# Kernel optimization log

Hardware: AMD Instinct MI355X
Metric: run time of the kernel (lower is better)

## Reference

```python
import jax, jax.numpy as jnp
import numpy as np

EPS = 1e-5

def _bn_relu(x, gamma, beta):
    # BatchNorm2d in training mode: biased batch stats over (B, H, W)
    mu = jnp.mean(x, axis=(0, 2, 3), keepdims=True)
    var = jnp.mean((x - mu) ** 2, axis=(0, 2, 3), keepdims=True)
    xh = (x - mu) * jax.lax.rsqrt(var + EPS)
    return jax.nn.relu(xh * gamma[None, :, None, None] + beta[None, :, None, None])

def setup_inputs() -> dict:
    key = jax.random.key(0)
    ks = jax.random.split(key, 16)
    B, N, D = 4, 256, 256            # in_channels = 2*D = 512
    feats = jax.random.normal(ks[0], (B, 1 + 2 * N, D), dtype=jnp.float32)
    def lin(k, o, c):
        return jax.random.normal(k, (o, c), dtype=jnp.float32) * (1.0 / np.sqrt(c))
    return {
        "feats": feats,
        "W1": lin(ks[1], 256, 512), "b1": jnp.zeros((256,), jnp.float32),
        "g1": jnp.ones((256,), jnp.float32), "be1": jnp.zeros((256,), jnp.float32),
        "W2": lin(ks[2], 128, 256), "b2": jnp.zeros((128,), jnp.float32),
        "g2": jnp.ones((128,), jnp.float32), "be2": jnp.zeros((128,), jnp.float32),
        "W3": lin(ks[3], 64, 128), "b3": jnp.zeros((64,), jnp.float32),
        "g3": jnp.ones((64,), jnp.float32), "be3": jnp.zeros((64,), jnp.float32),
        "W4": lin(ks[4], 1, 64), "b4": jnp.zeros((1,), jnp.float32),
    }

def reference(feats, W1, b1, g1, be1, W2, b2, g2, be2, W3, b3, g3, be3, W4, b4):
    B, T, Dfull = feats.shape
    f = feats[:, 1:]                                  # [B, 2N, D]
    N = f.shape[1] // 2
    D = f.shape[2]
    f = f.reshape(B, N, 2, D).mean(axis=2)            # [B, N, D]
    fc = jnp.transpose(f, (0, 2, 1))                  # [B, D, N]
    # conv1(cat(x, t)) fused: first D input channels see f_i, last D see f_j
    a = jnp.einsum('oc,bcn->bon', W1[:, :D], fc)      # [B, 256, N]
    bpart = jnp.einsum('oc,bcn->bon', W1[:, D:], fc)  # [B, 256, N]
    h = a[:, :, :, None] + bpart[:, :, None, :] + b1[None, :, None, None]  # [B,256,N,N]
    h = _bn_relu(h, g1, be1)
    h = jnp.einsum('oc,bcij->boij', W2, h) + b2[None, :, None, None]
    h = _bn_relu(h, g2, be2)
    h = jnp.einsum('oc,bcij->boij', W3, h) + b3[None, :, None, None]
    h = _bn_relu(h, g3, be3)
    h = jnp.einsum('oc,bcij->boij', W4, h) + b4[None, :, None, None]
    return h[:, 0]                                    # [B, N, N]
```

## Files before the change

### kernel.cpp

```cpp
#include <hip/hip_runtime.h>
#include <hip/hip_bf16.h>

#define EPS 1e-5f

typedef __attribute__((ext_vector_type(8))) short bf16x8;
typedef __attribute__((ext_vector_type(4))) float f32x4;

static constexpr size_t OFF_FT    = 0;
static constexpr size_t OFF_W1T   = 1048576;
static constexpr size_t OFF_W2B   = 1572864;
static constexpr size_t OFF_W3B   = 1638400;
static constexpr size_t OFF_S1    = 1654784;
static constexpr size_t OFF_T1    = 1655808;
static constexpr size_t OFF_S2    = 1658368;
static constexpr size_t OFF_T2    = 1658880;
static constexpr size_t OFF_S3    = 1659392;
static constexpr size_t OFF_T3    = 1659648;
static constexpr size_t OFF_ST2   = 1660928;
static constexpr size_t OFF_ST3   = 1669120;
static constexpr size_t OFF_ABT   = 1703936;
static constexpr size_t OFF_H2T   = 4194304;
static constexpr size_t OFF_P1    = OFF_H2T;
static constexpr size_t OFF_H3T   = 71303168;

static __device__ inline float bfu2f(unsigned int u16) {
    return __uint_as_float(u16 << 16);
}
static __device__ inline unsigned short f2bfu(float f) {
    unsigned int u = __float_as_uint(f);
    unsigned int r = u + 0x7fffu + ((u >> 16) & 1u);
    return (unsigned short)(r >> 16);
}
static __device__ inline unsigned int pkbf(float lo, float hi) {
    __hip_bfloat162 p = __float22bfloat162_rn(make_float2(lo, hi));
    return *reinterpret_cast<unsigned int*>(&p);
}

__global__ void k0_pairmean_T(const float* __restrict__ feats, float* __restrict__ fT) {
    __shared__ float s[64][65];
    int b = blockIdx.x >> 2;
    int n0 = (blockIdx.x & 3) * 64;
    int tid = threadIdx.x;
    const float* fb = feats + (size_t)b * 513 * 256;
    for (int c0 = 0; c0 < 256; c0 += 64) {
        for (int idx = tid; idx < 64 * 64; idx += 256) {
            int n = idx >> 6, c = idx & 63;
            const float* r = fb + (size_t)(1 + 2 * (n0 + n)) * 256 + c0 + c;
            s[n][c] = 0.5f * (r[0] + r[256]);
        }
        __syncthreads();
        for (int idx = tid; idx < 64 * 64; idx += 256) {
            int c = idx >> 6, n = idx & 63;
            fT[((size_t)b * 256 + c0 + c) * 256 + n0 + n] = s[n][c];
        }
        __syncthreads();
    }
}

__global__ void kt_prep(const float* __restrict__ W1, const float* __restrict__ W2,
                        const float* __restrict__ W3, float* __restrict__ W1T,
                        unsigned short* __restrict__ W2b, unsigned short* __restrict__ W3b) {
    int idx = blockIdx.x * 256 + threadIdx.x;
    if (idx < 131072) {
        int c = idx >> 9, o = idx & 511;
        W1T[idx] = (o < 256) ? W1[(size_t)o * 512 + c] : W1[(size_t)(o - 256) * 512 + 256 + c];
    } else if (idx < 163840) {
        int j = idx - 131072;
        W2b[j] = f2bfu(W2[j]);
    } else if (idx < 172032) {
        int j = idx - 163840;
        W3b[j] = f2bfu(W3[j]);
    }
}

__global__ __launch_bounds__(256) void k1_gemm(const float* __restrict__ W1T,
                                               const float* __restrict__ fT,
                                               float* __restrict__ abT,
                                               float2* __restrict__ part) {
    __shared__ float sW[64][68];
    __shared__ float sF[64][68];
    int tid = threadIdx.x;
    int b = blockIdx.x >> 2, n0 = (blockIdx.x & 3) * 64;
    int o0 = blockIdx.y * 64;
    int jq = tid & 15, og = tid >> 4;
    float acc[4][4] = {};
    for (int c0 = 0; c0 < 256; c0 += 64) {
        for (int idx = tid; idx < 64 * 64; idx += 256) {
            int c = idx >> 6, o = idx & 63;
            sW[c][o] = W1T[(size_t)(c0 + c) * 512 + o0 + o];
        }
        for (int idx = tid; idx < 64 * 64; idx += 256) {
            int c = idx >> 6, n = idx & 63;
            sF[c][n] = fT[((size_t)b * 256 + c0 + c) * 256 + n0 + n];
        }
        __syncthreads();
        #pragma unroll 8
        for (int c = 0; c < 64; ++c) {
            float4 rv = *(const float4*)&sF[c][jq * 4];
            float4 wv = *(const float4*)&sW[c][og * 4];
            float rr[4] = {rv.x, rv.y, rv.z, rv.w};
            float ww[4] = {wv.x, wv.y, wv.z, wv.w};
            #pragma unroll
            for (int m = 0; m < 4; ++m)
                #pragma unroll
                for (int w = 0; w < 4; ++w) acc[m][w] += ww[m] * rr[w];
        }
        __syncthreads();
    }
    for (int w = 0; w < 4; ++w) {
        int n = n0 + jq * 4 + w;
        float4 v = {acc[0][w], acc[1][w], acc[2][w], acc[3][w]};
        *(float4*)&abT[((size_t)(b * 256) + n) * 512 + o0 + og * 4] = v;
    }
    #pragma unroll
    for (int m = 0; m < 4; ++m) {
        float s = 0.f, q = 0.f;
        #pragma unroll
        for (int w = 0; w < 4; ++w) { float v = acc[m][w]; s += v; q += v * v; }
        #pragma unroll
        for (int off = 8; off; off >>= 1) { s += __shfl_down(s, off); q += __shfl_down(q, off); }
        if (jq == 0) part[(size_t)blockIdx.x * 512 + o0 + og * 4 + m] = make_float2(s, q);
    }
}

__global__ void k1b_stats(const float2* __restrict__ part, const float* __restrict__ g1,
                          const float* __restrict__ be1, float* __restrict__ s1,
                          float* __restrict__ t1) {
    __shared__ float Sl[4][512], Ql[4][512];
    int o = threadIdx.x;
    for (int b = 0; b < 4; ++b) {
        float s = 0.f, q = 0.f;
        #pragma unroll
        for (int nt = 0; nt < 4; ++nt) {
            float2 p = part[(size_t)(b * 4 + nt) * 512 + o];
            s += p.x; q += p.y;
        }
        Sl[b][o] = s; Ql[b][o] = q;
    }
    __syncthreads();
    if (o < 256) {
        float msum = 0.f, e2sum = 0.f;
        #pragma unroll
        for (int b = 0; b < 4; ++b) {
            float ma = Sl[b][o] * (1.f / 256.f), mb = Sl[b][o + 256] * (1.f / 256.f);
            msum += ma + mb;
            e2sum += Ql[b][o] * (1.f / 256.f) + Ql[b][o + 256] * (1.f / 256.f) + 2.f * ma * mb;
        }
        float m = msum * 0.25f, e2 = e2sum * 0.25f;
        float var = e2 - m * m;
        float s = g1[o] * rsqrtf(var + EPS);
        s1[o] = s;
        t1[o] = be1[o] - m * s;
    }
}

__global__ __launch_bounds__(256) void k2_mfma(const float* __restrict__ abT,
                                               const unsigned short* __restrict__ W2b,
                                               const float* __restrict__ s1,
                                               const float* __restrict__ t1,
                                               unsigned short* __restrict__ h2T,
                                               float* __restrict__ gS2,
                                               float* __restrict__ gQ2) {
    __shared__ __align__(16) char smem[39936];
    float* aaS = (float*)smem;
    float* ssS = (float*)(smem + 1024);
    unsigned short* sW = (unsigned short*)(smem + 2048);
    unsigned short* sB = (unsigned short*)(smem + 20480);
    float* sS = (float*)(smem + 38912);
    float* sQ = (float*)(smem + 39424);
    unsigned short* sT = (unsigned short*)smem;

    int tid = threadIdx.x;
    int j0 = blockIdx.x * 128, i = blockIdx.y, b = blockIdx.z;

    {
        float av = abT[((size_t)(b * 256 + i)) * 512 + tid];
        float s = s1[tid];
        aaS[tid] = fmaf(av, s, t1[tid]);
        ssS[tid] = s;
    }
    if (tid < 128) { sS[tid] = 0.f; sQ[tid] = 0.f; }
    __syncthreads();

    int lane = tid & 63, wv = tid >> 6;
    int wr = wv >> 1, wc = wv & 1;
    int lo = lane & 15, khi = lane >> 4;

    f32x4 acc[4][4] = {};
    const float* bpB = abT + ((size_t)(b * 256 + j0)) * 512 + 256;

    for (int c0 = 0; c0 < 256; c0 += 64) {
        #pragma unroll
        for (int k = 0; k < 4; ++k) {
            int f = tid + k * 256; int o = f >> 3, cs = f & 7;
            uint4 v = *(const uint4*)(W2b + o * 256 + c0 + cs * 8);
            *(uint4*)(sW + o * 72 + cs * 8) = v;
        }
        #pragma unroll
        for (int k = 0; k < 8; ++k) {
            int f = tid + k * 256; int j = f >> 4, cs = f & 15;
            float4 bp = *(const float4*)(bpB + (size_t)j * 512 + c0 + cs * 4);
            float4 a4 = *(const float4*)&aaS[c0 + cs * 4];
            float4 s4 = *(const float4*)&ssS[c0 + cs * 4];
            float r0 = fmaxf(fmaf(bp.x, s4.x, a4.x), 0.f);
            float r1 = fmaxf(fmaf(bp.y, s4.y, a4.y), 0.f);
            float r2 = fmaxf(fmaf(bp.z, s4.z, a4.z), 0.f);
            float r3 = fmaxf(fmaf(bp.w, s4.w, a4.w), 0.f);
            *(uint2*)(sB + j * 72 + cs * 4) = make_uint2(pkbf(r0, r1), pkbf(r2, r3));
        }
        __syncthreads();
        const unsigned short* aB = sW + (wr * 64 + lo) * 72 + khi * 8;
        const unsigned short* bB = sB + (wc * 64 + lo) * 72 + khi * 8;
        #pragma unroll
        for (int ks = 0; ks < 2; ++ks) {
            bf16x8 af[4], bfr[4];
            #pragma unroll
            for (int fm = 0; fm < 4; ++fm) af[fm] = *(const bf16x8*)(aB + fm * 16 * 72 + ks * 32);
            #pragma unroll
            for (int fn = 0; fn < 4; ++fn) bfr[fn] = *(const bf16x8*)(bB + fn * 16 * 72 + ks * 32);
            #pragma unroll
            for (int fm = 0; fm < 4; ++fm)
                #pragma unroll
                for (int fn = 0; fn < 4; ++fn)
                    acc[fm][fn] = __builtin_amdgcn_mfma_f32_16x16x32_bf16(af[fm], bfr[fn], acc[fm][fn], 0, 0, 0);
        }
        __syncthreads();
    }

    #pragma unroll
    for (int fm = 0; fm < 4; ++fm)
        #pragma unroll
        for (int r = 0; r < 4; ++r) {
            float s = 0.f, q = 0.f;
            #pragma unroll
            for (int fn = 0; fn < 4; ++fn) { float v = acc[fm][fn][r]; s += v; q += v * v; }
            #pragma unroll
            for (int off = 8; off; off >>= 1) { s += __shfl_down(s, off); q += __shfl_down(q, off); }
            if (lo == 0) {
                int o = wr * 64 + fm * 16 + khi * 4 + r;
                atomicAdd(&sS[o], s);
                atomicAdd(&sQ[o], q);
            }
        }
    __syncthreads();

    #pragma unroll
    for (int fm = 0; fm < 4; ++fm)
        #pragma unroll
        for (int fn = 0; fn < 4; ++fn) {
            int oq = wr * 64 + fm * 16 + khi * 4;
            int j  = wc * 64 + fn * 16 + lo;
            unsigned int u0 = pkbf(acc[fm][fn][0], acc[fm][fn][1]);
            unsigned int u1 = pkbf(acc[fm][fn][2], acc[fm][fn][3]);
            *(uint2*)(sT + j * 136 + oq) = make_uint2(u0, u1);
        }
    __syncthreads();
    {
        int jrow = tid >> 1, half = tid & 1;
        size_t gbase = (((size_t)(b * 256 + i)) * 256 + j0 + jrow) * 128 + half * 64;
        #pragma unroll
        for (int e = 0; e < 8; ++e) {
            uint4 v = *(const uint4*)(sT + jrow * 136 + half * 64 + e * 8);
            *(uint4*)(h2T + gbase + e * 8) = v;
        }
    }
    if (tid < 128) {
        int slot = (i & 7) * 128;
        atomicAdd(&gS2[slot + tid], sS[tid]);
        atomicAdd(&gQ2[slot + tid], sQ[tid]);
    }
}

__global__ void kbnparam(const float* __restrict__ gS, const float* __restrict__ gQ,
                         const float* __restrict__ g, const float* __restrict__ be,
                         float* __restrict__ s, float* __restrict__ t, int C, float invc) {
    int o = threadIdx.x;
    if (o < C) {
        float su = 0.f, qu = 0.f;
        #pragma unroll
        for (int k = 0; k < 8; ++k) { su += gS[k * C + o]; qu += gQ[k * C + o]; }
        float mean = su * invc;
        float var = qu * invc - mean * mean;
        float sc = g[o] * rsqrtf(var + EPS);
        s[o] = sc;
        t[o] = be[o] - mean * sc;
    }
}

__global__ __launch_bounds__(256) void k3_mfma(const unsigned short* __restrict__ h2T,
                                               const unsigned short* __restrict__ W3b,
                                               const float* __restrict__ s2,
                                               const float* __restrict__ t2,
                                               unsigned short* __restrict__ h3T,
                                               float* __restrict__ gS3,
                                               float* __restrict__ gQ3) {
    __shared__ __align__(16) char smem[39424];
    float* s2S = (float*)smem;
    float* t2S = (float*)(smem + 512);
    unsigned short* sW3 = (unsigned short*)(smem + 1024);
    unsigned short* sB  = (unsigned short*)(smem + 18432);
    float* sS = (float*)(smem + 38912);
    float* sQ = (float*)(smem + 39168);
    unsigned short* sT  = (unsigned short*)(smem + 1024);

    int tid = threadIdx.x;
    int i = blockIdx.x, b = blockIdx.y;
    if (tid < 128) { s2S[tid] = s2[tid]; t2S[tid] = t2[tid]; }
    if (tid < 64) { sS[tid] = 0.f; sQ[tid] = 0.f; }
    {
        int o = tid >> 2, qd = tid & 3;
        #pragma unroll
        for (int e = 0; e < 4; ++e) {
            uint4 v = *(const uint4*)(W3b + o * 128 + qd * 32 + e * 8);
            *(uint4*)(sW3 + o * 136 + qd * 32 + e * 8) = v;
        }
    }
    __syncthreads();

    int lane = tid & 63, wv = tid >> 6;
    int lo = lane & 15, khi = lane >> 4;

    f32x4 acc[4][4] = {};
    const unsigned short* src = h2T + (((size_t)(b * 256 + i)) * 256 + tid) * 128;

    for (int c0 = 0; c0 < 128; c0 += 32) {
        #pragma unroll
        for (int e = 0; e < 4; ++e) {
            uint4 v = *(const uint4*)(src + c0 + e * 8);
            int c = c0 + e * 8;
            float4 sa = *(const float4*)&s2S[c];
            float4 sb = *(const float4*)&s2S[c + 4];
            float4 ta = *(const float4*)&t2S[c];
            float4 tb = *(const float4*)&t2S[c + 4];
            float r0 = fmaxf(fmaf(bfu2f(v.x & 0xffffu), sa.x, ta.x), 0.f);
            float r1 = fmaxf(fmaf(bfu2f(v.x >> 16),     sa.y, ta.y), 0.f);
            float r2 = fmaxf(fmaf(bfu2f(v.y & 0xffffu), sa.z, ta.z), 0.f);
            float r3 = fmaxf(fmaf(bfu2f(v.y >> 16),     sa.w, ta.w), 0.f);
            float r4 = fmaxf(fmaf(bfu2f(v.z & 0xffffu), sb.x, tb.x), 0.f);
            float r5 = fmaxf(fmaf(bfu2f(v.z >> 16),     sb.y, tb.y), 0.f);
            float r6 = fmaxf(fmaf(bfu2f(v.w & 0xffffu), sb.z, tb.z), 0.f);
            float r7 = fmaxf(fmaf(bfu2f(v.w >> 16),     sb.w, tb.w), 0.f);
            *(uint4*)(sB + tid * 40 + e * 8) =
                make_uint4(pkbf(r0, r1), pkbf(r2, r3), pkbf(r4, r5), pkbf(r6, r7));
        }
        __syncthreads();
        bf16x8 af[4], bfr[4];
        #pragma unroll
        for (int fm = 0; fm < 4; ++fm)
            af[fm] = *(const bf16x8*)(sW3 + (fm * 16 + lo) * 136 + c0 + khi * 8);
        #pragma unroll
        for (int fn = 0; fn < 4; ++fn)
            bfr[fn] = *(const bf16x8*)(sB + (wv * 64 + fn * 16 + lo) * 40 + khi * 8);
        #pragma unroll
        for (int fm = 0; fm < 4; ++fm)
            #pragma unroll
            for (int fn = 0; fn < 4; ++fn)
                acc[fm][fn] = __builtin_amdgcn_mfma_f32_16x16x32_bf16(af[fm], bfr[fn], acc[fm][fn], 0, 0, 0);
        __syncthreads();
    }

    #pragma unroll
    for (int fm = 0; fm < 4; ++fm)
        #pragma unroll
        for (int r = 0; r < 4; ++r) {
            float s = 0.f, q = 0.f;
            #pragma unroll
            for (int fn = 0; fn < 4; ++fn) { float v = acc[fm][fn][r]; s += v; q += v * v; }
            #pragma unroll
            for (int off = 8; off; off >>= 1) { s += __shfl_down(s, off); q += __shfl_down(q, off); }
            if (lo == 0) {
                int o = fm * 16 + khi * 4 + r;
                atomicAdd(&sS[o], s);
                atomicAdd(&sQ[o], q);
            }
        }
    __syncthreads();

    #pragma unroll
    for (int fm = 0; fm < 4; ++fm)
        #pragma unroll
        for (int fn = 0; fn < 4; ++fn) {
            int oq = fm * 16 + khi * 4;
            int j  = wv * 64 + fn * 16 + lo;
            unsigned int u0 = pkbf(acc[fm][fn][0], acc[fm][fn][1]);
            unsigned int u1 = pkbf(acc[fm][fn][2], acc[fm][fn][3]);
            *(uint2*)(sT + j * 72 + oq) = make_uint2(u0, u1);
        }
    __syncthreads();
    {
        size_t gbase = (((size_t)(b * 256 + i)) * 256 + tid) * 64;
        #pragma unroll
        for (int e = 0; e < 8; ++e) {
            uint4 v = *(const uint4*)(sT + tid * 72 + e * 8);
            *(uint4*)(h3T + gbase + e * 8) = v;
        }
    }
    if (tid < 64) {
        int slot = (i & 7) * 64;
        atomicAdd(&gS3[slot + tid], sS[tid]);
        atomicAdd(&gQ3[slot + tid], sQ[tid]);
    }
}

__global__ __launch_bounds__(256) void k4_final(const unsigned short* __restrict__ h3T,
                                                const float* __restrict__ W4,
                                                const float* __restrict__ s3,
                                                const float* __restrict__ t3,
                                                const float* __restrict__ b4,
                                                float* __restrict__ out) {
    __shared__ __align__(16) char smem[37632];
    float* wS = (float*)smem;
    float* sS = (float*)(smem + 256);
    float* tS = (float*)(smem + 512);
    unsigned short* sL = (unsigned short*)(smem + 768);
    int tid = threadIdx.x;
    int i = blockIdx.x, b = blockIdx.y;
    if (tid < 64) { wS[tid] = W4[tid]; sS[tid] = s3[tid]; tS[tid] = t3[tid]; }
    const unsigned short* src = h3T + ((size_t)(b * 256 + i)) * 256 * 64;
    #pragma unroll
    for (int e = 0; e < 8; ++e) {
        int f = tid + 256 * e;
        uint4 v = *(const uint4*)(src + f * 8);
        *(uint4*)(sL + (f >> 3) * 72 + (f & 7) * 8) = v;
    }
    __syncthreads();
    float acc = 0.f;
    #pragma unroll
    for (int e = 0; e < 8; ++e) {
        uint4 v = *(const uint4*)(sL + tid * 72 + e * 8);
        unsigned int w[4] = {v.x, v.y, v.z, v.w};
        #pragma unroll
        for (int k = 0; k < 4; ++k) {
            int c = e * 8 + 2 * k;
            float f0 = bfu2f(w[k] & 0xffffu);
            float f1 = bfu2f(w[k] >> 16);
            acc += wS[c] * fmaxf(fmaf(f0, sS[c], tS[c]), 0.f);
            acc += wS[c + 1] * fmaxf(fmaf(f1, sS[c + 1], tS[c + 1]), 0.f);
        }
    }
    out[((size_t)(b * 256 + i)) * 256 + tid] = acc + b4[0];
}

extern "C" void kernel_launch(void* const* d_in, const int* in_sizes, int n_in,
                              void* d_out, int out_size, void* d_ws, size_t ws_size,
                              hipStream_t stream) {
    const float* feats = (const float*)d_in[0];
    const float* W1  = (const float*)d_in[1];
    const float* g1  = (const float*)d_in[3];
    const float* be1 = (const float*)d_in[4];
    const float* W2  = (const float*)d_in[5];
    const float* g2  = (const float*)d_in[7];
    const float* be2 = (const float*)d_in[8];
    const float* W3  = (const float*)d_in[9];
    const float* g3  = (const float*)d_in[11];
    const float* be3 = (const float*)d_in[12];
    const float* W4  = (const float*)d_in[13];
    const float* b4  = (const float*)d_in[14];

    char* ws = (char*)d_ws;
    float* fT   = (float*)(ws + OFF_FT);
    float* W1T  = (float*)(ws + OFF_W1T);
    unsigned short* W2b = (unsigned short*)(ws + OFF_W2B);
    unsigned short* W3b = (unsigned short*)(ws + OFF_W3B);
    float* abT  = (float*)(ws + OFF_ABT);
    float* s1   = (float*)(ws + OFF_S1);
    float* t1   = (float*)(ws + OFF_T1);
    float* gS2  = (float*)(ws + OFF_ST2);
    float* gQ2  = (float*)(ws + OFF_ST2 + 4096);
    float* gS3  = (float*)(ws + OFF_ST3);
    float* gQ3  = (float*)(ws + OFF_ST3 + 2048);
    float* s2 = (float*)(ws + OFF_S2);
    float* t2 = (float*)(ws + OFF_T2);
    float* s3 = (float*)(ws + OFF_S3);
    float* t3 = (float*)(ws + OFF_T3);
    float2* part = (float2*)(ws + OFF_P1);
    unsigned short* h2T = (unsigned short*)(ws + OFF_H2T);
    unsigned short* h3T = (unsigned short*)(ws + OFF_H3T);
    float* out = (float*)d_out;

    hipMemsetAsync(ws + OFF_ST2, 0, 12288, stream);

    k0_pairmean_T<<<16, 256, 0, stream>>>(feats, fT);
    kt_prep<<<672, 256, 0, stream>>>(W1, W2, W3, W1T, W2b, W3b);
    k1_gemm<<<dim3(16, 8), 256, 0, stream>>>(W1T, fT, abT, part);
    k1b_stats<<<1, 512, 0, stream>>>(part, g1, be1, s1, t1);
    k2_mfma<<<dim3(2, 256, 4), 256, 0, stream>>>(abT, W2b, s1, t1, h2T, gS2, gQ2);
    kbnparam<<<1, 128, 0, stream>>>(gS2, gQ2, g2, be2, s2, t2, 128, 1.f / 262144.f);
    k3_mfma<<<dim3(256, 4), 256, 0, stream>>>(h2T, W3b, s2, t2, h3T, gS3, gQ3);
    kbnparam<<<1, 64, 0, stream>>>(gS3, gQ3, g3, be3, s3, t3, 64, 1.f / 262144.f);
    k4_final<<<dim3(256, 4), 256, 0, stream>>>(h3T, W4, s3, t3, b4, out);
}
```

Before: 241.6 us.

## Double-buffer k2/k3 MFMA loops, load weights from global, split small kernels wider

The k2 and k3 MFMA kernels now double-buffer the BN+ReLU-transformed B tile in LDS. They prefetch the next chunk's activations and weight fragments into registers while the current MFMAs run, and they read weight fragments straight from global memory instead of staging them in shared memory. k3 is split over two j-halves for more blocks, and its LDS footprint shrinks, which should allow higher occupancy. k0 and k1 get more, smaller blocks to fill more CUs. The cost is more global weight traffic, which relies on L2 hits, plus extra register pressure from the prefetched data.

```diff
diff --git a/kernel.cpp b/kernel.cpp
--- a/kernel.cpp
+++ b/kernel.cpp
@@ -36,24 +36,46 @@
     return *reinterpret_cast<unsigned int*>(&p);
 }
 
-__global__ void k0_pairmean_T(const float* __restrict__ feats, float* __restrict__ fT) {
-    __shared__ float s[64][65];
-    int b = blockIdx.x >> 2;
-    int n0 = (blockIdx.x & 3) * 64;
+static __device__ __forceinline__ uint2 bnpk4(float4 fv, const float* aa, const float* ss, int c) {
+    float4 a4 = *(const float4*)(aa + c);
+    float4 s4 = *(const float4*)(ss + c);
+    float r0 = fmaxf(fmaf(fv.x, s4.x, a4.x), 0.f);
+    float r1 = fmaxf(fmaf(fv.y, s4.y, a4.y), 0.f);
+    float r2 = fmaxf(fmaf(fv.z, s4.z, a4.z), 0.f);
+    float r3 = fmaxf(fmaf(fv.w, s4.w, a4.w), 0.f);
+    return make_uint2(pkbf(r0, r1), pkbf(r2, r3));
+}
+static __device__ __forceinline__ uint2 bn2pk4(uint2 v, const float* ss, const float* tt, int c) {
+    float4 s4 = *(const float4*)(ss + c);
+    float4 t4 = *(const float4*)(tt + c);
+    float r0 = fmaxf(fmaf(bfu2f(v.x & 0xffffu), s4.x, t4.x), 0.f);
+    float r1 = fmaxf(fmaf(bfu2f(v.x >> 16),     s4.y, t4.y), 0.f);
+    float r2 = fmaxf(fmaf(bfu2f(v.y & 0xffffu), s4.z, t4.z), 0.f);
+    float r3 = fmaxf(fmaf(bfu2f(v.y >> 16),     s4.w, t4.w), 0.f);
+    return make_uint2(pkbf(r0, r1), pkbf(r2, r3));
+}
+
+__global__ __launch_bounds__(256) void k0_pairmean_T(const float* __restrict__ feats,
+                                                     float* __restrict__ fT) {
+    __shared__ float s[32][65];
+    int bx = blockIdx.x;
+    int b = bx >> 5, nt = (bx >> 2) & 7, ct = bx & 3;
+    int n0 = nt * 32, c0 = ct * 64;
     int tid = threadIdx.x;
     const float* fb = feats + (size_t)b * 513 * 256;
-    for (int c0 = 0; c0 < 256; c0 += 64) {
-        for (int idx = tid; idx < 64 * 64; idx += 256) {
-            int n = idx >> 6, c = idx & 63;
-            const float* r = fb + (size_t)(1 + 2 * (n0 + n)) * 256 + c0 + c;
-            s[n][c] = 0.5f * (r[0] + r[256]);
-        }
-        __syncthreads();
-        for (int idx = tid; idx < 64 * 64; idx += 256) {
-            int c = idx >> 6, n = idx & 63;
-            fT[((size_t)b * 256 + c0 + c) * 256 + n0 + n] = s[n][c];
-        }
-        __syncthreads();
+    #pragma unroll
+    for (int k = 0; k < 8; ++k) {
+        int idx = tid + k * 256;
+        int n = idx >> 6, c = idx & 63;
+        const float* r = fb + (size_t)(1 + 2 * (n0 + n)) * 256 + c0 + c;
+        s[n][c] = 0.5f * (r[0] + r[256]);
+    }
+    __syncthreads();
+    #pragma unroll
+    for (int k = 0; k < 8; ++k) {
+        int idx = tid + k * 256;
+        int c = idx >> 5, n = idx & 31;
+        fT[((size_t)(b * 256) + c0 + c) * 256 + n0 + n] = s[n][c];
     }
 }
 
@@ -77,49 +99,55 @@
                                                const float* __restrict__ fT,
                                                float* __restrict__ abT,
                                                float2* __restrict__ part) {
-    __shared__ float sW[64][68];
+    __shared__ float sW[64][36];
     __shared__ float sF[64][68];
     int tid = threadIdx.x;
-    int b = blockIdx.x >> 2, n0 = (blockIdx.x & 3) * 64;
-    int o0 = blockIdx.y * 64;
-    int jq = tid & 15, og = tid >> 4;
-    float acc[4][4] = {};
+    int bx = blockIdx.x;
+    int b = bx >> 2, n0 = (bx & 3) * 64;
+    int o0 = blockIdx.y * 32;
+    int og = tid >> 4, jq = tid & 15;
+    float acc[2][4] = {};
     for (int c0 = 0; c0 < 256; c0 += 64) {
-        for (int idx = tid; idx < 64 * 64; idx += 256) {
-            int c = idx >> 6, o = idx & 63;
+        #pragma unroll
+        for (int k = 0; k < 8; ++k) {
+            int idx = tid + k * 256;
+            int c = idx >> 5, o = idx & 31;
             sW[c][o] = W1T[(size_t)(c0 + c) * 512 + o0 + o];
         }
-        for (int idx = tid; idx < 64 * 64; idx += 256) {
+        #pragma unroll
+        for (int k = 0; k < 16; ++k) {
+            int idx = tid + k * 256;
             int c = idx >> 6, n = idx & 63;
-            sF[c][n] = fT[((size_t)b * 256 + c0 + c) * 256 + n0 + n];
+            sF[c][n] = fT[((size_t)(b * 256) + c0 + c) * 256 + n0 + n];
         }
         __syncthreads();
         #pragma unroll 8
         for (int c = 0; c < 64; ++c) {
             float4 rv = *(const float4*)&sF[c][jq * 4];
-            float4 wv = *(const float4*)&sW[c][og * 4];
+            float2 wv = *(const float2*)&sW[c][og * 2];
             float rr[4] = {rv.x, rv.y, rv.z, rv.w};
-            float ww[4] = {wv.x, wv.y, wv.z, wv.w};
             #pragma unroll
-            for (int m = 0; m < 4; ++m)
-                #pragma unroll
-                for (int w = 0; w < 4; ++w) acc[m][w] += ww[m] * rr[w];
+            for (int w = 0; w < 4; ++w) {
+                acc[0][w] = fmaf(wv.x, rr[w], acc[0][w]);
+                acc[1][w] = fmaf(wv.y, rr[w], acc[1][w]);
+            }
         }
         __syncthreads();
     }
+    #pragma unroll
     for (int w = 0; w < 4; ++w) {
         int n = n0 + jq * 4 + w;
-        float4 v = {acc[0][w], acc[1][w], acc[2][w], acc[3][w]};
-        *(float4*)&abT[((size_t)(b * 256) + n) * 512 + o0 + og * 4] = v;
-    }
-    #pragma unroll
-    for (int m = 0; m < 4; ++m) {
+        *(float2*)&abT[((size_t)(b * 256) + n) * 512 + o0 + og * 2] =
+            make_float2(acc[0][w], acc[1][w]);
+    }
+    #pragma unroll
+    for (int m = 0; m < 2; ++m) {
         float s = 0.f, q = 0.f;
         #pragma unroll
         for (int w = 0; w < 4; ++w) { float v = acc[m][w]; s += v; q += v * v; }
         #pragma unroll
         for (int off = 8; off; off >>= 1) { s += __shfl_down(s, off); q += __shfl_down(q, off); }
-        if (jq == 0) part[(size_t)blockIdx.x * 512 + o0 + og * 4 + m] = make_float2(s, q);
+        if (jq == 0) part[(size_t)bx * 512 + o0 + og * 2 + m] = make_float2(s, q);
     }
 }
 
@@ -161,14 +189,14 @@
                                                unsigned short* __restrict__ h2T,
                                                float* __restrict__ gS2,
                                                float* __restrict__ gQ2) {
-    __shared__ __align__(16) char smem[39936];
+    __shared__ __align__(16) char smem[23552];
     float* aaS = (float*)smem;
     float* ssS = (float*)(smem + 1024);
-    unsigned short* sW = (unsigned short*)(smem + 2048);
-    unsigned short* sB = (unsigned short*)(smem + 20480);
-    float* sS = (float*)(smem + 38912);
-    float* sQ = (float*)(smem + 39424);
-    unsigned short* sT = (unsigned short*)smem;
+    float* sS  = (float*)(smem + 2048);
+    float* sQ  = (float*)(smem + 2560);
+    unsigned short* sB0 = (unsigned short*)(smem + 3072);
+    unsigned short* sB1 = (unsigned short*)(smem + 13312);
+    unsigned short* sT  = (unsigned short*)(smem + 3072);
 
     int tid = threadIdx.x;
     int j0 = blockIdx.x * 128, i = blockIdx.y, b = blockIdx.z;
@@ -185,46 +213,73 @@
     int lane = tid & 63, wv = tid >> 6;
     int wr = wv >> 1, wc = wv & 1;
     int lo = lane & 15, khi = lane >> 4;
+    int jr = tid >> 1, half = tid & 1;
+
+    const float* bpRow = abT + ((size_t)(b * 256 + j0 + jr)) * 512 + 256 + half * 16;
+    const unsigned short* wBase = W2b + (wr * 64 + lo) * 256 + khi * 8;
 
     f32x4 acc[4][4] = {};
-    const float* bpB = abT + ((size_t)(b * 256 + j0)) * 512 + 256;
-
-    for (int c0 = 0; c0 < 256; c0 += 64) {
-        #pragma unroll
-        for (int k = 0; k < 4; ++k) {
-            int f = tid + k * 256; int o = f >> 3, cs = f & 7;
-            uint4 v = *(const uint4*)(W2b + o * 256 + c0 + cs * 8);
-            *(uint4*)(sW + o * 72 + cs * 8) = v;
-        }
-        #pragma unroll
-        for (int k = 0; k < 8; ++k) {
-            int f = tid + k * 256; int j = f >> 4, cs = f & 15;
-            float4 bp = *(const float4*)(bpB + (size_t)j * 512 + c0 + cs * 4);
-            float4 a4 = *(const float4*)&aaS[c0 + cs * 4];
-            float4 s4 = *(const float4*)&ssS[c0 + cs * 4];
-            float r0 = fmaxf(fmaf(bp.x, s4.x, a4.x), 0.f);
-            float r1 = fmaxf(fmaf(bp.y, s4.y, a4.y), 0.f);
-            float r2 = fmaxf(fmaf(bp.z, s4.z, a4.z), 0.f);
-            float r3 = fmaxf(fmaf(bp.w, s4.w, a4.w), 0.f);
-            *(uint2*)(sB + j * 72 + cs * 4) = make_uint2(pkbf(r0, r1), pkbf(r2, r3));
+    bf16x8 af0, af1, af2, af3;
+
+    {
+        int c = half * 16;
+        float4 f0 = *(const float4*)(bpRow + 0);
+        float4 f1 = *(const float4*)(bpRow + 4);
+        float4 f2 = *(const float4*)(bpRow + 8);
+        float4 f3 = *(const float4*)(bpRow + 12);
+        uint2 p0 = bnpk4(f0, aaS, ssS, c);
+        uint2 p1 = bnpk4(f1, aaS, ssS, c + 4);
+        uint2 p2 = bnpk4(f2, aaS, ssS, c + 8);
+        uint2 p3 = bnpk4(f3, aaS, ssS, c + 12);
+        *(uint4*)(sB0 + jr * 40 + half * 16)     = make_uint4(p0.x, p0.y, p1.x, p1.y);
+        *(uint4*)(sB0 + jr * 40 + half * 16 + 8) = make_uint4(p2.x, p2.y, p3.x, p3.y);
+    }
+    af0 = *(const bf16x8*)(wBase);
+    af1 = *(const bf16x8*)(wBase + 4096);
+    af2 = *(const bf16x8*)(wBase + 8192);
+    af3 = *(const bf16x8*)(wBase + 12288);
+    __syncthreads();
+
+    unsigned short* curB = sB0;
+    unsigned short* nxtB = sB1;
+    #pragma unroll 2
+    for (int k = 0; k < 8; ++k) {
+        int c0 = k * 32;
+        float4 f0, f1, f2, f3;
+        bf16x8 an0, an1, an2, an3;
+        if (k < 7) {
+            f0 = *(const float4*)(bpRow + c0 + 32);
+            f1 = *(const float4*)(bpRow + c0 + 36);
+            f2 = *(const float4*)(bpRow + c0 + 40);
+            f3 = *(const float4*)(bpRow + c0 + 44);
+            an0 = *(const bf16x8*)(wBase + c0 + 32);
+            an1 = *(const bf16x8*)(wBase + 4096 + c0 + 32);
+            an2 = *(const bf16x8*)(wBase + 8192 + c0 + 32);
+            an3 = *(const bf16x8*)(wBase + 12288 + c0 + 32);
+        }
+        bf16x8 bfr[4];
+        #pragma unroll
+        for (int fn = 0; fn < 4; ++fn)
+            bfr[fn] = *(const bf16x8*)(curB + (wc * 64 + fn * 16 + lo) * 40 + khi * 8);
+        #pragma unroll
+        for (int fn = 0; fn < 4; ++fn) {
+            acc[0][fn] = __builtin_amdgcn_mfma_f32_16x16x32_bf16(af0, bfr[fn], acc[0][fn], 0, 0, 0);
+            acc[1][fn] = __builtin_amdgcn_mfma_f32_16x16x32_bf16(af1, bfr[fn], acc[1][fn], 0, 0, 0);
+            acc[2][fn] = __builtin_amdgcn_mfma_f32_16x16x32_bf16(af2, bfr[fn], acc[2][fn], 0, 0, 0);
+            acc[3][fn] = __builtin_amdgcn_mfma_f32_16x16x32_bf16(af3, bfr[fn], acc[3][fn], 0, 0, 0);
+        }
+        if (k < 7) {
+            int cn = c0 + 32 + half * 16;
+            uint2 p0 = bnpk4(f0, aaS, ssS, cn);
+            uint2 p1 = bnpk4(f1, aaS, ssS, cn + 4);
+            uint2 p2 = bnpk4(f2, aaS, ssS, cn + 8);
+            uint2 p3 = bnpk4(f3, aaS, ssS, cn + 12);
+            *(uint4*)(nxtB + jr * 40 + half * 16)     = make_uint4(p0.x, p0.y, p1.x, p1.y);
+            *(uint4*)(nxtB + jr * 40 + half * 16 + 8) = make_uint4(p2.x, p2.y, p3.x, p3.y);
+            af0 = an0; af1 = an1; af2 = an2; af3 = an3;
         }
         __syncthreads();
-        const unsigned short* aB = sW + (wr * 64 + lo) * 72 + khi * 8;
-        const unsigned short* bB = sB + (wc * 64 + lo) * 72 + khi * 8;
-        #pragma unroll
-        for (int ks = 0; ks < 2; ++ks) {
-            bf16x8 af[4], bfr[4];
-            #pragma unroll
-            for (int fm = 0; fm < 4; ++fm) af[fm] = *(const bf16x8*)(aB + fm * 16 * 72 + ks * 32);
-            #pragma unroll
-            for (int fn = 0; fn < 4; ++fn) bfr[fn] = *(const bf16x8*)(bB + fn * 16 * 72 + ks * 32);
-            #pragma unroll
-            for (int fm = 0; fm < 4; ++fm)
-                #pragma unroll
-                for (int fn = 0; fn < 4; ++fn)
-                    acc[fm][fn] = __builtin_amdgcn_mfma_f32_16x16x32_bf16(af[fm], bfr[fn], acc[fm][fn], 0, 0, 0);
-        }
-        __syncthreads();
+        unsigned short* t = curB; curB = nxtB; nxtB = t;
     }
 
     #pragma unroll
@@ -242,26 +297,28 @@
                 atomicAdd(&sQ[o], q);
             }
         }
-    __syncthreads();
-
-    #pragma unroll
-    for (int fm = 0; fm < 4; ++fm)
-        #pragma unroll
-        for (int fn = 0; fn < 4; ++fn) {
-            int oq = wr * 64 + fm * 16 + khi * 4;
-            int j  = wc * 64 + fn * 16 + lo;
-            unsigned int u0 = pkbf(acc[fm][fn][0], acc[fm][fn][1]);
-            unsigned int u1 = pkbf(acc[fm][fn][2], acc[fm][fn][3]);
-            *(uint2*)(sT + j * 136 + oq) = make_uint2(u0, u1);
-        }
-    __syncthreads();
-    {
-        int jrow = tid >> 1, half = tid & 1;
-        size_t gbase = (((size_t)(b * 256 + i)) * 256 + j0 + jrow) * 128 + half * 64;
-        #pragma unroll
-        for (int e = 0; e < 8; ++e) {
-            uint4 v = *(const uint4*)(sT + jrow * 136 + half * 64 + e * 8);
-            *(uint4*)(h2T + gbase + e * 8) = v;
+
+    #pragma unroll
+    for (int rr = 0; rr < 2; ++rr) {
+        __syncthreads();
+        if (wr == rr) {
+            #pragma unroll
+            for (int fm = 0; fm < 4; ++fm)
+                #pragma unroll
+                for (int fn = 0; fn < 4; ++fn) {
+                    int oq = fm * 16 + khi * 4;
+                    int j  = wc * 64 + fn * 16 + lo;
+                    *(uint2*)(sT + j * 72 + oq) =
+                        make_uint2(pkbf(acc[fm][fn][0], acc[fm][fn][1]),
+                                   pkbf(acc[fm][fn][2], acc[fm][fn][3]));
+                }
+        }
+        __syncthreads();
+        size_t g = (((size_t)(b * 256 + i)) * 256 + j0 + jr) * 128 + rr * 64 + half * 32;
+        #pragma unroll
+        for (int e = 0; e < 4; ++e) {
+            uint4 v = *(const uint4*)(sT + jr * 72 + half * 32 + e * 8);
+            *(uint4*)(h2T + g + e * 8) = v;
         }
     }
     if (tid < 128) {
@@ -294,69 +351,86 @@
                                                unsigned short* __restrict__ h3T,
                                                float* __restrict__ gS3,
                                                float* __restrict__ gQ3) {
-    __shared__ __align__(16) char smem[39424];
+    __shared__ __align__(16) char smem[22016];
     float* s2S = (float*)smem;
     float* t2S = (float*)(smem + 512);
-    unsigned short* sW3 = (unsigned short*)(smem + 1024);
-    unsigned short* sB  = (unsigned short*)(smem + 18432);
-    float* sS = (float*)(smem + 38912);
-    float* sQ = (float*)(smem + 39168);
-    unsigned short* sT  = (unsigned short*)(smem + 1024);
+    float* sS  = (float*)(smem + 1024);
+    float* sQ  = (float*)(smem + 1280);
+    unsigned short* sB0 = (unsigned short*)(smem + 1536);
+    unsigned short* sB1 = (unsigned short*)(smem + 11776);
+    unsigned short* sT  = (unsigned short*)(smem + 1536);
 
     int tid = threadIdx.x;
-    int i = blockIdx.x, b = blockIdx.y;
+    int j0 = blockIdx.x * 128, i = blockIdx.y, b = blockIdx.z;
     if (tid < 128) { s2S[tid] = s2[tid]; t2S[tid] = t2[tid]; }
     if (tid < 64) { sS[tid] = 0.f; sQ[tid] = 0.f; }
-    {
-        int o = tid >> 2, qd = tid & 3;
-        #pragma unroll
-        for (int e = 0; e < 4; ++e) {
-            uint4 v = *(const uint4*)(W3b + o * 128 + qd * 32 + e * 8);
-            *(uint4*)(sW3 + o * 136 + qd * 32 + e * 8) = v;
-        }
-    }
     __syncthreads();
 
     int lane = tid & 63, wv = tid >> 6;
     int lo = lane & 15, khi = lane >> 4;
-
-    f32x4 acc[4][4] = {};
-    const unsigned short* src = h2T + (((size_t)(b * 256 + i)) * 256 + tid) * 128;
-
-    for (int c0 = 0; c0 < 128; c0 += 32) {
-        #pragma unroll
-        for (int e = 0; e < 4; ++e) {
-            uint4 v = *(const uint4*)(src + c0 + e * 8);
-            int c = c0 + e * 8;
-            float4 sa = *(const float4*)&s2S[c];
-            float4 sb = *(const float4*)&s2S[c + 4];
-            float4 ta = *(const float4*)&t2S[c];
-            float4 tb = *(const float4*)&t2S[c + 4];
-            float r0 = fmaxf(fmaf(bfu2f(v.x & 0xffffu), sa.x, ta.x), 0.f);
-            float r1 = fmaxf(fmaf(bfu2f(v.x >> 16),     sa.y, ta.y), 0.f);
-            float r2 = fmaxf(fmaf(bfu2f(v.y & 0xffffu), sa.z, ta.z), 0.f);
-            float r3 = fmaxf(fmaf(bfu2f(v.y >> 16),     sa.w, ta.w), 0.f);
-            float r4 = fmaxf(fmaf(bfu2f(v.z & 0xffffu), sb.x, tb.x), 0.f);
-            float r5 = fmaxf(fmaf(bfu2f(v.z >> 16),     sb.y, tb.y), 0.f);
-            float r6 = fmaxf(fmaf(bfu2f(v.w & 0xffffu), sb.z, tb.z), 0.f);
-            float r7 = fmaxf(fmaf(bfu2f(v.w >> 16),     sb.w, tb.w), 0.f);
-            *(uint4*)(sB + tid * 40 + e * 8) =
-                make_uint4(pkbf(r0, r1), pkbf(r2, r3), pkbf(r4, r5), pkbf(r6, r7));
+    int jr = tid >> 1, half = tid & 1;
+
+    const unsigned short* srcRow = h2T + (((size_t)(b * 256 + i)) * 256 + j0 + jr) * 128 + half * 16;
+    const unsigned short* wBase = W3b + lo * 128 + khi * 8;
+
+    f32x4 acc[4][2] = {};
+    bf16x8 af0, af1, af2, af3;
+
+    {
+        int c = half * 16;
+        uint4 v0 = *(const uint4*)(srcRow);
+        uint4 v1 = *(const uint4*)(srcRow + 8);
+        uint2 p0 = bn2pk4(make_uint2(v0.x, v0.y), s2S, t2S, c);
+        uint2 p1 = bn2pk4(make_uint2(v0.z, v0.w), s2S, t2S, c + 4);
+        uint2 p2 = bn2pk4(make_uint2(v1.x, v1.y), s2S, t2S, c + 8);
+        uint2 p3 = bn2pk4(make_uint2(v1.z, v1.w), s2S, t2S, c + 12);
+        *(uint4*)(sB0 + jr * 40 + half * 16)     = make_uint4(p0.x, p0.y, p1.x, p1.y);
+        *(uint4*)(sB0 + jr * 40 + half * 16 + 8) = make_uint4(p2.x, p2.y, p3.x, p3.y);
+    }
+    af0 = *(const bf16x8*)(wBase);
+    af1 = *(const bf16x8*)(wBase + 2048);
+    af2 = *(const bf16x8*)(wBase + 4096);
+    af3 = *(const bf16x8*)(wBase + 6144);
+    __syncthreads();
+
+    unsigned short* curB = sB0;
+    unsigned short* nxtB = sB1;
+    #pragma unroll 2
+    for (int k = 0; k < 4; ++k) {
+        int c0 = k * 32;
+        uint4 v0, v1;
+        bf16x8 an0, an1, an2, an3;
+        if (k < 3) {
+            v0 = *(const uint4*)(srcRow + c0 + 32);
+            v1 = *(const uint4*)(srcRow + c0 + 40);
+            an0 = *(const bf16x8*)(wBase + c0 + 32);
+            an1 = *(const bf16x8*)(wBase + 2048 + c0 + 32);
+            an2 = *(const bf16x8*)(wBase + 4096 + c0 + 32);
+            an3 = *(const bf16x8*)(wBase + 6144 + c0 + 32);
+        }
+        bf16x8 bfr[2];
+        #pragma unroll
+        for (int fn = 0; fn < 2; ++fn)
+            bfr[fn] = *(const bf16x8*)(curB + (wv * 32 + fn * 16 + lo) * 40 + khi * 8);
+        #pragma unroll
+        for (int fn = 0; fn < 2; ++fn) {
+            acc[0][fn] = __builtin_amdgcn_mfma_f32_16x16x32_bf16(af0, bfr[fn], acc[0][fn], 0, 0, 0);
+            acc[1][fn] = __builtin_amdgcn_mfma_f32_16x16x32_bf16(af1, bfr[fn], acc[1][fn], 0, 0, 0);
+            acc[2][fn] = __builtin_amdgcn_mfma_f32_16x16x32_bf16(af2, bfr[fn], acc[2][fn], 0, 0, 0);
+            acc[3][fn] = __builtin_amdgcn_mfma_f32_16x16x32_bf16(af3, bfr[fn], acc[3][fn], 0, 0, 0);
+        }
+        if (k < 3) {
+            int cn = c0 + 32 + half * 16;
+            uint2 p0 = bn2pk4(make_uint2(v0.x, v0.y), s2S, t2S, cn);
+            uint2 p1 = bn2pk4(make_uint2(v0.z, v0.w), s2S, t2S, cn + 4);
+            uint2 p2 = bn2pk4(make_uint2(v1.x, v1.y), s2S, t2S, cn + 8);
+            uint2 p3 = bn2pk4(make_uint2(v1.z, v1.w), s2S, t2S, cn + 12);
+            *(uint4*)(nxtB + jr * 40 + half * 16)     = make_uint4(p0.x, p0.y, p1.x, p1.y);
+            *(uint4*)(nxtB + jr * 40 + half * 16 + 8) = make_uint4(p2.x, p2.y, p3.x, p3.y);
+            af0 = an0; af1 = an1; af2 = an2; af3 = an3;
         }
         __syncthreads();
-        bf16x8 af[4], bfr[4];
-        #pragma unroll
-        for (int fm = 0; fm < 4; ++fm)
-            af[fm] = *(const bf16x8*)(sW3 + (fm * 16 + lo) * 136 + c0 + khi * 8);
-        #pragma unroll
-        for (int fn = 0; fn < 4; ++fn)
-            bfr[fn] = *(const bf16x8*)(sB + (wv * 64 + fn * 16 + lo) * 40 + khi * 8);
-        #pragma unroll
-        for (int fm = 0; fm < 4; ++fm)
-            #pragma unroll
-            for (int fn = 0; fn < 4; ++fn)
-                acc[fm][fn] = __builtin_amdgcn_mfma_f32_16x16x32_bf16(af[fm], bfr[fn], acc[fm][fn], 0, 0, 0);
-        __syncthreads();
+        unsigned short* t = curB; curB = nxtB; nxtB = t;
     }
 
     #pragma unroll
@@ -365,7 +439,7 @@
         for (int r = 0; r < 4; ++r) {
             float s = 0.f, q = 0.f;
             #pragma unroll
-            for (int fn = 0; fn < 4; ++fn) { float v = acc[fm][fn][r]; s += v; q += v * v; }
+            for (int fn = 0; fn < 2; ++fn) { float v = acc[fm][fn][r]; s += v; q += v * v; }
             #pragma unroll
             for (int off = 8; off; off >>= 1) { s += __shfl_down(s, off); q += __shfl_down(q, off); }
             if (lo == 0) {
@@ -379,20 +453,20 @@
     #pragma unroll
     for (int fm = 0; fm < 4; ++fm)
         #pragma unroll
-        for (int fn = 0; fn < 4; ++fn) {
+        for (int fn = 0; fn < 2; ++fn) {
             int oq = fm * 16 + khi * 4;
-            int j  = wv * 64 + fn * 16 + lo;
-            unsigned int u0 = pkbf(acc[fm][fn][0], acc[fm][fn][1]);
-            unsigned int u1 = pkbf(acc[fm][fn][2], acc[fm][fn][3]);
-            *(uint2*)(sT + j * 72 + oq) = make_uint2(u0, u1);
+            int j  = wv * 32 + fn * 16 + lo;
+            *(uint2*)(sT + j * 72 + oq) =
+                make_uint2(pkbf(acc[fm][fn][0], acc[fm][fn][1]),
+                           pkbf(acc[fm][fn][2], acc[fm][fn][3]));
         }
     __syncthreads();
     {
-        size_t gbase = (((size_t)(b * 256 + i)) * 256 + tid) * 64;
-        #pragma unroll
-        for (int e = 0; e < 8; ++e) {
-            uint4 v = *(const uint4*)(sT + tid * 72 + e * 8);
-            *(uint4*)(h3T + gbase + e * 8) = v;
+        size_t g = (((size_t)(b * 256 + i)) * 256 + j0 + jr) * 64 + half * 32;
+        #pragma unroll
+        for (int e = 0; e < 4; ++e) {
+            uint4 v = *(const uint4*)(sT + jr * 72 + half * 32 + e * 8);
+            *(uint4*)(h3T + g + e * 8) = v;
         }
     }
     if (tid < 64) {
@@ -480,13 +554,13 @@
 
     hipMemsetAsync(ws + OFF_ST2, 0, 12288, stream);
 
-    k0_pairmean_T<<<16, 256, 0, stream>>>(feats, fT);
+    k0_pairmean_T<<<128, 256, 0, stream>>>(feats, fT);
     kt_prep<<<672, 256, 0, stream>>>(W1, W2, W3, W1T, W2b, W3b);
-    k1_gemm<<<dim3(16, 8), 256, 0, stream>>>(W1T, fT, abT, part);
+    k1_gemm<<<dim3(16, 16), 256, 0, stream>>>(W1T, fT, abT, part);
     k1b_stats<<<1, 512, 0, stream>>>(part, g1, be1, s1, t1);
     k2_mfma<<<dim3(2, 256, 4), 256, 0, stream>>>(abT, W2b, s1, t1, h2T, gS2, gQ2);
     kbnparam<<<1, 128, 0, stream>>>(gS2, gQ2, g2, be2, s2, t2, 128, 1.f / 262144.f);
-    k3_mfma<<<dim3(256, 4), 256, 0, stream>>>(h2T, W3b, s2, t2, h3T, gS3, gQ3);
+    k3_mfma<<<dim3(2, 256, 4), 256, 0, stream>>>(h2T, W3b, s2, t2, h3T, gS3, gQ3);
     kbnparam<<<1, 64, 0, stream>>>(gS3, gQ3, g3, be3, s3, t3, 64, 1.f / 262144.f);
     k4_final<<<dim3(256, 4), 256, 0, stream>>>(h3T, W4, s3, t3, b4, out);
 }
```

Measured after the change: 244.1 us. Within noise of the previous version (+1.0%).
